# Performance work log

Measured on AMD Instinct MI355X. Metric: run time of the kernel, lower is better.

The kernel has to match this reference:

```python
import jax, jax.numpy as jnp
import numpy as np

BETA = 0.25  # codebook loss weight


def setup_inputs() -> dict:
    key = jax.random.key(0)
    k1, k2 = jax.random.split(key)
    B, C, D = 32768, 4096, 128
    x = jax.random.normal(k1, (B, D), dtype=jnp.float32)
    codes = jax.random.normal(k2, (1, C, D), dtype=jnp.float32)
    return {"x": x, "codes": codes}


def reference(x, codes):
    # x: (B, D), codes: (1, C, D). l2 metric, spherical_norm=False, STE training path
    # (dead-code reinit branch is a no-op on first forward since unused_count==0).
    c = codes[0]  # (C, D)
    x_sq = jnp.sum(x * x, axis=-1, keepdims=True)           # (B, 1)
    c_sq = jnp.sum(c * c, axis=-1)                          # (C,)
    xc = jnp.einsum('bd,cd->bc', x, c)                      # (B, C)
    distances = x_sq + c_sq[None, :] - 2.0 * xc             # (B, C)
    indices = jnp.argmin(distances, axis=-1)                # (B,)
    quantized = c[indices]                                  # (B, D) codebook gather
    # straight-through estimator output
    quantized_out = x + jax.lax.stop_gradient(quantized - x)
    # loss_commit: distance(x, stop_grad(q)); loss_codebook: distance(stop_grad(x), q)
    q_sg = jax.lax.stop_gradient(quantized)
    x_sg = jax.lax.stop_gradient(x)
    loss_commit = jnp.mean(jnp.sum((x - q_sg) ** 2, axis=-1))
    loss_codebook = jnp.mean(jnp.sum((x_sg - quantized) ** 2, axis=-1))
    loss = loss_commit + BETA * loss_codebook
    return quantized_out, indices, loss
```

## Files before the change

kernel.cpp:

```cpp
#include <hip/hip_runtime.h>
#include <float.h>

#define B_ROWS 32768
#define C_CODES 4096
#define DDIM 128
#define MB 128
#define NCHUNKS 4
#define CCHUNK 1024
#define CTILE 64
#define NTILES 16
#define ROWB 256

typedef __attribute__((ext_vector_type(8))) short short8;
typedef __attribute__((ext_vector_type(16))) float f32x16;
using half8 = __attribute__((ext_vector_type(8))) _Float16;
typedef unsigned int u32;
typedef unsigned short u16;
typedef unsigned long long u64;

__device__ __forceinline__ u16 f2h(float f) {
    return __builtin_bit_cast(u16, (_Float16)f);
}

__device__ __forceinline__ void gl2lds16(const void* g, void* l) {
    __builtin_amdgcn_global_load_lds(
        (const __attribute__((address_space(1))) u32*)g,
        (__attribute__((address_space(3))) u32*)l, 16, 0, 0);
}

__global__ void prep_codes(const float* __restrict__ codes, u16* __restrict__ Bbig,
                           float* __restrict__ csqh) {
    const int w = threadIdx.x >> 6, lane = threadIdx.x & 63;
    const int c = blockIdx.x * 4 + w;
    const float2 v = ((const float2*)(codes + (size_t)c * DDIM))[lane];
    ushort2 b; b.x = f2h(v.x); b.y = f2h(v.y);
    const int sw = (c & 15) << 4;
    *(ushort2*)((char*)Bbig + (size_t)c * ROWB + ((lane * 4) ^ sw)) = b;
    float s = v.x * v.x + v.y * v.y;
    #pragma unroll
    for (int off = 32; off; off >>= 1) s += __shfl_xor(s, off);
    if (lane == 0) csqh[c] = 0.5f * s;
}

__global__ void transpose_codes(const float* __restrict__ codes, float* __restrict__ codesT) {
    const int g = blockIdx.x * 256 + threadIdx.x;
    const int d = g & 127;
    const int cg = g >> 7;
    float buf[32];
    #pragma unroll
    for (int k = 0; k < 32; ++k)
        buf[k] = codes[(size_t)(cg * 32 + k) * DDIM + d];
    #pragma unroll
    for (int i = 0; i < 8; ++i) {
        float4 v;
        v.x = buf[i * 4]; v.y = buf[i * 4 + 1]; v.z = buf[i * 4 + 2]; v.w = buf[i * 4 + 3];
        *(float4*)&codesT[(size_t)d * C_CODES + cg * 32 + i * 4] = v;
    }
}

__global__ __launch_bounds__(256, 2)
void gemm_top2(const float* __restrict__ x, const u16* __restrict__ Bbig,
               const float* __restrict__ csqh,
               float* __restrict__ pb1, float* __restrict__ pb2,
               int* __restrict__ pi1, float* __restrict__ xsq_ws) {
    __shared__ char smem[32768 + 4096 + 1024];
    char* const Astage = smem;
    float* const csq_l = (float*)(smem + 32768);
    float* const xsqArr = (float*)(smem + 36864);

    const int tid = threadIdx.x;
    const int lane = tid & 63;
    const int w = tid >> 6;
    const int blkrow = blockIdx.x * MB;
    const int cbase = blockIdx.y * CCHUNK;

    {
        const float4 v = ((const float4*)(csqh + cbase))[tid];
        float4 n; n.x = -v.x; n.y = -v.y; n.z = -v.z; n.w = -v.w;
        ((float4*)csq_l)[tid] = n;
    }
    {
        const int r = tid >> 1, h = tid & 1;
        const float4* xp = (const float4*)(x + (size_t)(blkrow + r) * DDIM + h * 64);
        char* Arow = Astage + r * ROWB;
        const int sw = (r & 15) << 4;
        float ss = 0.f;
        #pragma unroll
        for (int i = 0; i < 16; ++i) {
            const float4 v = xp[i];
            ss += v.x * v.x + v.y * v.y + v.z * v.z + v.w * v.w;
            uint2 pk;
            pk.x = (u32)f2h(v.x) | ((u32)f2h(v.y) << 16);
            pk.y = (u32)f2h(v.z) | ((u32)f2h(v.w) << 16);
            *(uint2*)(Arow + ((h * 128 + i * 8) ^ sw)) = pk;
        }
        xsqArr[tid] = ss;
    }
    __syncthreads();

    const int col0 = lane & 31;
    const int khalf = (lane >> 5) << 4;
    half8 afr[8];
    {
        const int arow = w * 32 + col0;
        const char* Ab = Astage + arow * ROWB;
        const int swa = (arow & 15) << 4;
        #pragma unroll
        for (int ks = 0; ks < 8; ++ks)
            afr[ks] = *(const half8*)(Ab + ((ks * 32 + khalf) ^ swa));
    }
    __syncthreads();

    {
        const char* src = (const char*)Bbig + (size_t)cbase * ROWB;
        #pragma unroll
        for (int r = 0; r < 4; ++r)
            gl2lds16(src + r * 4096 + w * 1024 + lane * 16, smem + r * 4096 + w * 1024);
    }
    __syncthreads();

    float b1v[16], b2v[16]; int b1i[16];
    #pragma unroll
    for (int r = 0; r < 16; ++r) { b1v[r] = -FLT_MAX; b2v[r] = -FLT_MAX; b1i[r] = 0; }

    const int swb = (col0 & 15) << 4;

    for (int t = 0; t < NTILES; ++t) {
        if (t + 1 < NTILES) {
            char* dbuf = smem + ((t + 1) & 1) * 16384;
            const char* src = (const char*)Bbig + (size_t)(cbase + (t + 1) * CTILE) * ROWB;
            #pragma unroll
            for (int r = 0; r < 4; ++r)
                gl2lds16(src + r * 4096 + w * 1024 + lane * 16, dbuf + r * 4096 + w * 1024);
        }
        const char* Bl = smem + (t & 1) * 16384 + col0 * ROWB;

        const float cs0 = csq_l[t * CTILE + col0];
        const float cs1 = csq_l[t * CTILE + 32 + col0];
        f32x16 acc0, acc1;
        #pragma unroll
        for (int i = 0; i < 16; ++i) { acc0[i] = cs0; acc1[i] = cs1; }
        __builtin_amdgcn_s_setprio(1);
        #pragma unroll
        for (int ks = 0; ks < 8; ++ks) {
            const int z = (ks * 32 + khalf) ^ swb;
            const half8 bf0 = *(const half8*)(Bl + z);
            const half8 bf1 = *(const half8*)(Bl + 8192 + z);
            acc0 = __builtin_amdgcn_mfma_f32_32x32x16_f16(afr[ks], bf0, acc0, 0, 0, 0);
            acc1 = __builtin_amdgcn_mfma_f32_32x32x16_f16(afr[ks], bf1, acc1, 0, 0, 0);
        }
        __builtin_amdgcn_s_setprio(0);
        const int idx0 = cbase + t * CTILE + col0;
        const int idx1 = idx0 + 32;
        #pragma unroll
        for (int r = 0; r < 16; ++r) {
            const float s0 = acc0[r];
            const float s1 = acc1[r];
            const float m2a = __builtin_amdgcn_fmed3f(b1v[r], b2v[r], s0);
            const int   nia = (s0 > b1v[r]) ? idx0 : b1i[r];
            const float n1a = fmaxf(b1v[r], s0);
            b2v[r] = __builtin_amdgcn_fmed3f(n1a, m2a, s1);
            b1i[r] = (s1 > n1a) ? idx1 : nia;
            b1v[r] = fmaxf(n1a, s1);
        }
        __syncthreads();
    }

    #pragma unroll
    for (int off = 1; off <= 16; off <<= 1) {
        #pragma unroll
        for (int r = 0; r < 16; ++r) {
            const float o1 = __shfl_xor(b1v[r], off);
            const int   oi = __shfl_xor(b1i[r], off);
            const float o2 = __shfl_xor(b2v[r], off);
            const float lo = fminf(b1v[r], o1);
            const float nb2 = fmaxf(lo, fmaxf(b2v[r], o2));
            const bool take = (o1 > b1v[r]) || (o1 == b1v[r] && oi < b1i[r]);
            if (take) { b1v[r] = o1; b1i[r] = oi; }
            b2v[r] = nb2;
        }
    }
    if (col0 == 0) {
        const int hi = lane >> 5;
        #pragma unroll
        for (int r = 0; r < 16; ++r) {
            const int rloc = w * 32 + (r & 3) + 8 * (r >> 2) + 4 * hi;
            const int grow = blkrow + rloc;
            const size_t o = (size_t)blockIdx.y * B_ROWS + grow;
            pb1[o] = b1v[r]; pb2[o] = b2v[r]; pi1[o] = b1i[r];
            if (blockIdx.y == 0)
                xsq_ws[grow] = xsqArr[2 * rloc] + xsqArr[2 * rloc + 1];
        }
    }
}

__global__ void select_flag(const float* __restrict__ pb1, const float* __restrict__ pb2,
                            const int* __restrict__ pi1, const float* __restrict__ xsq_ws,
                            int* __restrict__ idxf, int* __restrict__ list, int* __restrict__ cnt,
                            u64* __restrict__ amax64) {
    const int r = blockIdx.x * 256 + threadIdx.x;
    float b1 = pb1[r], b2 = pb2[r]; int bi = pi1[r];
    #pragma unroll
    for (int c = 1; c < NCHUNKS; ++c) {
        const float o1 = pb1[(size_t)c * B_ROWS + r], o2 = pb2[(size_t)c * B_ROWS + r];
        const int oi = pi1[(size_t)c * B_ROWS + r];
        const float lo = fminf(b1, o1);
        b2 = fmaxf(lo, fmaxf(b2, o2));
        const bool take = (o1 > b1) || (o1 == b1 && oi < bi);
        if (take) { b1 = o1; bi = oi; }
    }
    idxf[r] = bi;
    const float margin = 0.004f * sqrtf(xsq_ws[r]) + 0.008f;
    const bool flag = (b1 - b2) < margin;
    const unsigned long long m = __ballot(flag);
    const int lane = threadIdx.x & 63;
    int base = 0;
    const int nw = __popcll(m);
    if (lane == 0 && nw) base = atomicAdd(cnt, nw);
    base = __shfl(base, 0);
    if (flag) {
        const int pos = base + (int)__popcll(m & ((1ull << lane) - 1ull));
        list[pos] = r;
        amax64[pos] = 0ull;
    }
}

__global__ __launch_bounds__(256)
void recheck2(const float* __restrict__ x, const float* __restrict__ codesT,
              const float* __restrict__ csqh, const int* __restrict__ list,
              const int* __restrict__ cnt, u64* __restrict__ amax64) {
    __shared__ float xT[128][8];
    __shared__ u64 warr[4][8];
    const int tid = threadIdx.x;
    const int lane = tid & 63, w = tid >> 6;
    const int n = *cnt;
    if (n == 0) return;
    const int ntasks = ((n + 7) >> 3) << 3;

    for (int task = blockIdx.x; task < ntasks; task += gridDim.x) {
        const int slotbase = (task >> 3) << 3;
        const int ch = task & 7;
        __syncthreads();
        #pragma unroll
        for (int k = 0; k < 4; ++k) {
            const int i = tid + k * 256;
            const int d = i & 127, j = i >> 7;
            const int slot = min(slotbase + j, n - 1);
            xT[d][j] = x[(size_t)list[slot] * DDIM + d];
        }
        __syncthreads();

        const int c0 = ch * 512 + tid;
        const int c1 = c0 + 256;
        float acc[2][8][4];
        #pragma unroll
        for (int cc = 0; cc < 2; ++cc)
            #pragma unroll
            for (int r = 0; r < 8; ++r)
                #pragma unroll
                for (int p = 0; p < 4; ++p) acc[cc][r][p] = 0.f;

        for (int d4 = 0; d4 < 32; ++d4) {
            #pragma unroll
            for (int p = 0; p < 4; ++p) {
                const int d = d4 * 4 + p;
                const float cv0 = codesT[(size_t)d * C_CODES + c0];
                const float cv1 = codesT[(size_t)d * C_CODES + c1];
                const float4 xa = *(const float4*)&xT[d][0];
                const float4 xb = *(const float4*)&xT[d][4];
                acc[0][0][p] = fmaf(cv0, xa.x, acc[0][0][p]);
                acc[0][1][p] = fmaf(cv0, xa.y, acc[0][1][p]);
                acc[0][2][p] = fmaf(cv0, xa.z, acc[0][2][p]);
                acc[0][3][p] = fmaf(cv0, xa.w, acc[0][3][p]);
                acc[0][4][p] = fmaf(cv0, xb.x, acc[0][4][p]);
                acc[0][5][p] = fmaf(cv0, xb.y, acc[0][5][p]);
                acc[0][6][p] = fmaf(cv0, xb.z, acc[0][6][p]);
                acc[0][7][p] = fmaf(cv0, xb.w, acc[0][7][p]);
                acc[1][0][p] = fmaf(cv1, xa.x, acc[1][0][p]);
                acc[1][1][p] = fmaf(cv1, xa.y, acc[1][1][p]);
                acc[1][2][p] = fmaf(cv1, xa.z, acc[1][2][p]);
                acc[1][3][p] = fmaf(cv1, xa.w, acc[1][3][p]);
                acc[1][4][p] = fmaf(cv1, xb.x, acc[1][4][p]);
                acc[1][5][p] = fmaf(cv1, xb.y, acc[1][5][p]);
                acc[1][6][p] = fmaf(cv1, xb.z, acc[1][6][p]);
                acc[1][7][p] = fmaf(cv1, xb.w, acc[1][7][p]);
            }
        }

        const float cq0 = csqh[c0], cq1 = csqh[c1];
        #pragma unroll
        for (int r = 0; r < 8; ++r) {
            const float s0 = (acc[0][r][0] + acc[0][r][1]) + (acc[0][r][2] + acc[0][r][3]) - cq0;
            const float s1 = (acc[1][r][0] + acc[1][r][1]) + (acc[1][r][2] + acc[1][r][3]) - cq1;
            const float sb = (s1 > s0) ? s1 : s0;
            const int ib = (s1 > s0) ? c1 : c0;
            u32 su = __float_as_uint(sb);
            su ^= (sb < 0.f) ? 0xFFFFFFFFu : 0x80000000u;
            u64 key = ((u64)su << 32) | (u32)(4095 - ib);
            #pragma unroll
            for (int off = 1; off < 64; off <<= 1) {
                const u64 o = __shfl_xor(key, off);
                key = (o > key) ? o : key;
            }
            if (lane == 0) warr[w][r] = key;
        }
        __syncthreads();
        if (tid < 8) {
            const u64 k01 = warr[0][tid] > warr[1][tid] ? warr[0][tid] : warr[1][tid];
            const u64 k23 = warr[2][tid] > warr[3][tid] ? warr[2][tid] : warr[3][tid];
            const u64 k = k01 > k23 ? k01 : k23;
            atomicMax(&amax64[min(slotbase + tid, n - 1)], k);
        }
    }
}

__global__ void merge_flag(const int* __restrict__ list, const int* __restrict__ cnt,
                           const u64* __restrict__ amax64, int* __restrict__ idxf) {
    const int n = *cnt;
    for (int i = blockIdx.x * 256 + threadIdx.x; i < n; i += gridDim.x * 256)
        idxf[list[i]] = 4095 - (int)(amax64[i] & 0xFFFFFFFFull);
}

__global__ void finalize(const float* __restrict__ x, const float* __restrict__ codes,
                         const int* __restrict__ idxf, float* __restrict__ qout,
                         float* __restrict__ idxout, float* __restrict__ partials) {
    __shared__ float ls[4];
    const int w = threadIdx.x >> 6, lane = threadIdx.x & 63;
    const int rb = blockIdx.x * 16 + w * 4;
    float wsum = 0.f;
    #pragma unroll
    for (int j = 0; j < 4; ++j) {
        const int r = rb + j;
        const int bi = idxf[r];
        const float2 xv = ((const float2*)(x + (size_t)r * DDIM))[lane];
        const float2 cv = ((const float2*)(codes + (size_t)bi * DDIM))[lane];
        ((float2*)(qout + (size_t)r * DDIM))[lane] = cv;
        if (lane == 0) idxout[r] = (float)bi;
        const float dx = xv.x - cv.x, dy = xv.y - cv.y;
        wsum += dx * dx + dy * dy;
    }
    #pragma unroll
    for (int off = 32; off; off >>= 1) wsum += __shfl_xor(wsum, off);
    if (lane == 0) ls[w] = wsum;
    __syncthreads();
    if (threadIdx.x == 0) partials[blockIdx.x] = (ls[0] + ls[1]) + (ls[2] + ls[3]);
}

__global__ void loss_reduce(const float* __restrict__ partials, float* __restrict__ loss) {
    __shared__ float ls[4];
    const int tid = threadIdx.x, w = tid >> 6, lane = tid & 63;
    float s = 0.f;
    for (int i = tid; i < 2048; i += 256) s += partials[i];
    #pragma unroll
    for (int off = 32; off; off >>= 1) s += __shfl_xor(s, off);
    if (lane == 0) ls[w] = s;
    __syncthreads();
    if (tid == 0) *loss = ((ls[0] + ls[1]) + (ls[2] + ls[3])) * (1.25f / (float)B_ROWS);
}

extern "C" void kernel_launch(void* const* d_in, const int* in_sizes, int n_in,
                              void* d_out, int out_size, void* d_ws, size_t ws_size,
                              hipStream_t stream) {
    const float* x = (const float*)d_in[0];
    const float* codes = (const float*)d_in[1];

    float* out = (float*)d_out;
    float* qout = out;
    float* idxout = out + (size_t)B_ROWS * DDIM;
    float* loss = idxout + B_ROWS;

    float* codesT = qout;

    char* ws = (char*)d_ws;
    u16* Bbig     = (u16*)ws;
    float* csqh   = (float*)(ws + 1048576);
    float* pb1    = (float*)(ws + 1064960);
    float* pb2    = (float*)(ws + 1589248);
    int* pi1      = (int*)(ws + 2113536);
    float* xsq_ws = (float*)(ws + 2637824);
    int* idxf     = (int*)(ws + 2768896);
    int* list     = (int*)(ws + 2899968);
    int* cnt      = (int*)(ws + 3031040);
    float* partials = (float*)(ws + 3031168);
    u64* amax64   = (u64*)(ws + 3039360);

    hipMemsetAsync(cnt, 0, 4, stream);
    prep_codes<<<C_CODES / 4, 256, 0, stream>>>(codes, Bbig, csqh);
    transpose_codes<<<64, 256, 0, stream>>>(codes, codesT);
    gemm_top2<<<dim3(B_ROWS / MB, NCHUNKS), 256, 0, stream>>>(x, Bbig, csqh, pb1, pb2, pi1, xsq_ws);
    select_flag<<<B_ROWS / 256, 256, 0, stream>>>(pb1, pb2, pi1, xsq_ws, idxf, list, cnt, amax64);
    recheck2<<<2048, 256, 0, stream>>>(x, codesT, csqh, list, cnt, amax64);
    merge_flag<<<64, 256, 0, stream>>>(list, cnt, amax64, idxf);
    finalize<<<B_ROWS / 16, 256, 0, stream>>>(x, codes, idxf, qout, idxout, partials);
    loss_reduce<<<1, 256, 0, stream>>>(partials, loss);
}
```

Baseline: 129.9 us.

## Deepen GEMM B-tile pipeline to 4 stages and halve codebook chunks

The distance GEMM now walks 32-code half-tiles through a 4-slot LDS ring with prefetch distance 2. It uses explicit vmcnt waits plus raw s_barrier instead of a full __syncthreads per 64-code tile. The codebook is split into 2 chunks of 2048 instead of 4, which halves the partial top-2 writes and the select_flag merge work but also halves grid parallelism. Per-row x-squared partials are written straight to global memory and summed in select_flag, dropping the LDS staging array. Risks are less MFMA interleaving with one accumulator per wave, fewer blocks, and correctness depending on the hand-placed waitcnt counts.

```diff
diff --git a/kernel.cpp b/kernel.cpp
--- a/kernel.cpp
+++ b/kernel.cpp
@@ -5,13 +5,11 @@
 #define C_CODES 4096
 #define DDIM 128
 #define MB 128
-#define NCHUNKS 4
-#define CCHUNK 1024
-#define CTILE 64
-#define NTILES 16
+#define NCHUNKS 2
+#define CCHUNK 2048
+#define NH 64
 #define ROWB 256
 
-typedef __attribute__((ext_vector_type(8))) short short8;
 typedef __attribute__((ext_vector_type(16))) float f32x16;
 using half8 = __attribute__((ext_vector_type(8))) _Float16;
 typedef unsigned int u32;
@@ -62,11 +60,10 @@
 void gemm_top2(const float* __restrict__ x, const u16* __restrict__ Bbig,
                const float* __restrict__ csqh,
                float* __restrict__ pb1, float* __restrict__ pb2,
-               int* __restrict__ pi1, float* __restrict__ xsq_ws) {
-    __shared__ char smem[32768 + 4096 + 1024];
+               int* __restrict__ pi1, float* __restrict__ xsq2) {
+    __shared__ char smem[32768 + 8192];
     char* const Astage = smem;
     float* const csq_l = (float*)(smem + 32768);
-    float* const xsqArr = (float*)(smem + 36864);
 
     const int tid = threadIdx.x;
     const int lane = tid & 63;
@@ -75,9 +72,13 @@
     const int cbase = blockIdx.y * CCHUNK;
 
     {
-        const float4 v = ((const float4*)(csqh + cbase))[tid];
-        float4 n; n.x = -v.x; n.y = -v.y; n.z = -v.z; n.w = -v.w;
-        ((float4*)csq_l)[tid] = n;
+        const float4* cs = (const float4*)(csqh + cbase);
+        #pragma unroll
+        for (int j = 0; j < 2; ++j) {
+            const float4 v = cs[j * 256 + tid];
+            float4 n; n.x = -v.x; n.y = -v.y; n.z = -v.z; n.w = -v.w;
+            ((float4*)csq_l)[j * 256 + tid] = n;
+        }
     }
     {
         const int r = tid >> 1, h = tid & 1;
@@ -94,7 +95,7 @@
             pk.y = (u32)f2h(v.z) | ((u32)f2h(v.w) << 16);
             *(uint2*)(Arow + ((h * 128 + i * 8) ^ sw)) = pk;
         }
-        xsqArr[tid] = ss;
+        if (blockIdx.y == 0) xsq2[blkrow * 2 + tid] = ss;
     }
     __syncthreads();
 
@@ -113,11 +114,13 @@
 
     {
         const char* src = (const char*)Bbig + (size_t)cbase * ROWB;
-        #pragma unroll
-        for (int r = 0; r < 4; ++r)
-            gl2lds16(src + r * 4096 + w * 1024 + lane * 16, smem + r * 4096 + w * 1024);
-    }
-    __syncthreads();
+        gl2lds16(src +         w * 1024 + lane * 16, smem +         w * 1024);
+        gl2lds16(src +  4096 + w * 1024 + lane * 16, smem +  4096 + w * 1024);
+        gl2lds16(src +  8192 + w * 1024 + lane * 16, smem +  8192 + w * 1024);
+        gl2lds16(src + 12288 + w * 1024 + lane * 16, smem + 12288 + w * 1024);
+    }
+    asm volatile("s_waitcnt vmcnt(2)" ::: "memory");
+    __builtin_amdgcn_s_barrier();
 
     float b1v[16], b2v[16]; int b1i[16];
     #pragma unroll
@@ -125,45 +128,38 @@
 
     const int swb = (col0 & 15) << 4;
 
-    for (int t = 0; t < NTILES; ++t) {
-        if (t + 1 < NTILES) {
-            char* dbuf = smem + ((t + 1) & 1) * 16384;
-            const char* src = (const char*)Bbig + (size_t)(cbase + (t + 1) * CTILE) * ROWB;
-            #pragma unroll
-            for (int r = 0; r < 4; ++r)
-                gl2lds16(src + r * 4096 + w * 1024 + lane * 16, dbuf + r * 4096 + w * 1024);
-        }
-        const char* Bl = smem + (t & 1) * 16384 + col0 * ROWB;
-
-        const float cs0 = csq_l[t * CTILE + col0];
-        const float cs1 = csq_l[t * CTILE + 32 + col0];
-        f32x16 acc0, acc1;
-        #pragma unroll
-        for (int i = 0; i < 16; ++i) { acc0[i] = cs0; acc1[i] = cs1; }
+    for (int h = 0; h < NH; ++h) {
+        if (h + 2 < NH) {
+            char* dbuf = smem + ((h + 2) & 3) * 8192;
+            const char* src = (const char*)Bbig + (size_t)(cbase + (h + 2) * 32) * ROWB;
+            gl2lds16(src +        w * 1024 + lane * 16, dbuf +        w * 1024);
+            gl2lds16(src + 4096 + w * 1024 + lane * 16, dbuf + 4096 + w * 1024);
+        }
+        const char* Bl = smem + (h & 3) * 8192 + col0 * ROWB;
+
+        const float cs0 = csq_l[h * 32 + col0];
+        f32x16 acc;
+        #pragma unroll
+        for (int i = 0; i < 16; ++i) acc[i] = cs0;
         __builtin_amdgcn_s_setprio(1);
         #pragma unroll
         for (int ks = 0; ks < 8; ++ks) {
-            const int z = (ks * 32 + khalf) ^ swb;
-            const half8 bf0 = *(const half8*)(Bl + z);
-            const half8 bf1 = *(const half8*)(Bl + 8192 + z);
-            acc0 = __builtin_amdgcn_mfma_f32_32x32x16_f16(afr[ks], bf0, acc0, 0, 0, 0);
-            acc1 = __builtin_amdgcn_mfma_f32_32x32x16_f16(afr[ks], bf1, acc1, 0, 0, 0);
+            const half8 bf = *(const half8*)(Bl + ((ks * 32 + khalf) ^ swb));
+            acc = __builtin_amdgcn_mfma_f32_32x32x16_f16(afr[ks], bf, acc, 0, 0, 0);
         }
         __builtin_amdgcn_s_setprio(0);
-        const int idx0 = cbase + t * CTILE + col0;
-        const int idx1 = idx0 + 32;
+        const int idx0 = cbase + h * 32 + col0;
         #pragma unroll
         for (int r = 0; r < 16; ++r) {
-            const float s0 = acc0[r];
-            const float s1 = acc1[r];
-            const float m2a = __builtin_amdgcn_fmed3f(b1v[r], b2v[r], s0);
-            const int   nia = (s0 > b1v[r]) ? idx0 : b1i[r];
-            const float n1a = fmaxf(b1v[r], s0);
-            b2v[r] = __builtin_amdgcn_fmed3f(n1a, m2a, s1);
-            b1i[r] = (s1 > n1a) ? idx1 : nia;
-            b1v[r] = fmaxf(n1a, s1);
-        }
-        __syncthreads();
+            const float s0 = acc[r];
+            const float m2 = __builtin_amdgcn_fmed3f(b1v[r], b2v[r], s0);
+            b1i[r] = (s0 > b1v[r]) ? idx0 : b1i[r];
+            b1v[r] = fmaxf(b1v[r], s0);
+            b2v[r] = m2;
+        }
+        if (h + 2 < NH) { asm volatile("s_waitcnt vmcnt(2)" ::: "memory"); }
+        else            { asm volatile("s_waitcnt vmcnt(0)" ::: "memory"); }
+        __builtin_amdgcn_s_barrier();
     }
 
     #pragma unroll
@@ -188,14 +184,12 @@
             const int grow = blkrow + rloc;
             const size_t o = (size_t)blockIdx.y * B_ROWS + grow;
             pb1[o] = b1v[r]; pb2[o] = b2v[r]; pi1[o] = b1i[r];
-            if (blockIdx.y == 0)
-                xsq_ws[grow] = xsqArr[2 * rloc] + xsqArr[2 * rloc + 1];
         }
     }
 }
 
 __global__ void select_flag(const float* __restrict__ pb1, const float* __restrict__ pb2,
-                            const int* __restrict__ pi1, const float* __restrict__ xsq_ws,
+                            const int* __restrict__ pi1, const float* __restrict__ xsq2,
                             int* __restrict__ idxf, int* __restrict__ list, int* __restrict__ cnt,
                             u64* __restrict__ amax64) {
     const int r = blockIdx.x * 256 + threadIdx.x;
@@ -210,7 +204,8 @@
         if (take) { b1 = o1; bi = oi; }
     }
     idxf[r] = bi;
-    const float margin = 0.004f * sqrtf(xsq_ws[r]) + 0.008f;
+    const float xsq = xsq2[2 * r] + xsq2[2 * r + 1];
+    const float margin = 0.004f * sqrtf(xsq) + 0.008f;
     const bool flag = (b1 - b2) < margin;
     const unsigned long long m = __ballot(flag);
     const int lane = threadIdx.x & 63;
@@ -375,20 +370,20 @@
     u16* Bbig     = (u16*)ws;
     float* csqh   = (float*)(ws + 1048576);
     float* pb1    = (float*)(ws + 1064960);
-    float* pb2    = (float*)(ws + 1589248);
-    int* pi1      = (int*)(ws + 2113536);
-    float* xsq_ws = (float*)(ws + 2637824);
-    int* idxf     = (int*)(ws + 2768896);
-    int* list     = (int*)(ws + 2899968);
-    int* cnt      = (int*)(ws + 3031040);
-    float* partials = (float*)(ws + 3031168);
-    u64* amax64   = (u64*)(ws + 3039360);
+    float* pb2    = (float*)(ws + 1327104);
+    int* pi1      = (int*)(ws + 1589248);
+    float* xsq2   = (float*)(ws + 1851392);
+    int* idxf     = (int*)(ws + 2113536);
+    int* list     = (int*)(ws + 2244608);
+    int* cnt      = (int*)(ws + 2375680);
+    float* partials = (float*)(ws + 2375808);
+    u64* amax64   = (u64*)(ws + 2384000);
 
     hipMemsetAsync(cnt, 0, 4, stream);
     prep_codes<<<C_CODES / 4, 256, 0, stream>>>(codes, Bbig, csqh);
     transpose_codes<<<64, 256, 0, stream>>>(codes, codesT);
-    gemm_top2<<<dim3(B_ROWS / MB, NCHUNKS), 256, 0, stream>>>(x, Bbig, csqh, pb1, pb2, pi1, xsq_ws);
-    select_flag<<<B_ROWS / 256, 256, 0, stream>>>(pb1, pb2, pi1, xsq_ws, idxf, list, cnt, amax64);
+    gemm_top2<<<dim3(B_ROWS / MB, NCHUNKS), 256, 0, stream>>>(x, Bbig, csqh, pb1, pb2, pi1, xsq2);
+    select_flag<<<B_ROWS / 256, 256, 0, stream>>>(pb1, pb2, pi1, xsq2, idxf, list, cnt, amax64);
     recheck2<<<2048, 256, 0, stream>>>(x, codesT, csqh, list, cnt, amax64);
     merge_flag<<<64, 256, 0, stream>>>(list, cnt, amax64, idxf);
     finalize<<<B_ROWS / 16, 256, 0, stream>>>(x, codes, idxf, qout, idxout, partials);
```

New measurement: 120.4 us. -7.3%, faster.

## Precompute fp16 swizzled x once in fused prep kernel; async-load it in GEMM

Applied to the files above, without the earlier changes.

Merges prep_codes, transpose_codes and a new x-to-fp16 conversion into one launch. The conversion writes swizzled fp16 rows and per-half squared norms into scratch space inside the output buffer. gemm_top2 then streams the pre-converted A tile into LDS with global_load_lds instead of reading fp32 x and converting it in each of the 4 chunk blocks. This removes repeated conversion work and a kernel launch, but adds an extra global write and read of the fp16 x (8 MB) and places scratch data in the output region, which later kernels must overwrite.

```diff
diff --git a/kernel.cpp b/kernel.cpp
--- a/kernel.cpp
+++ b/kernel.cpp
@@ -11,7 +11,6 @@
 #define NTILES 16
 #define ROWB 256
 
-typedef __attribute__((ext_vector_type(8))) short short8;
 typedef __attribute__((ext_vector_type(16))) float f32x16;
 using half8 = __attribute__((ext_vector_type(8))) _Float16;
 typedef unsigned int u32;
@@ -28,61 +27,41 @@
         (__attribute__((address_space(3))) u32*)l, 16, 0, 0);
 }
 
-__global__ void prep_codes(const float* __restrict__ codes, u16* __restrict__ Bbig,
-                           float* __restrict__ csqh) {
-    const int w = threadIdx.x >> 6, lane = threadIdx.x & 63;
-    const int c = blockIdx.x * 4 + w;
-    const float2 v = ((const float2*)(codes + (size_t)c * DDIM))[lane];
-    ushort2 b; b.x = f2h(v.x); b.y = f2h(v.y);
-    const int sw = (c & 15) << 4;
-    *(ushort2*)((char*)Bbig + (size_t)c * ROWB + ((lane * 4) ^ sw)) = b;
-    float s = v.x * v.x + v.y * v.y;
-    #pragma unroll
-    for (int off = 32; off; off >>= 1) s += __shfl_xor(s, off);
-    if (lane == 0) csqh[c] = 0.5f * s;
-}
-
-__global__ void transpose_codes(const float* __restrict__ codes, float* __restrict__ codesT) {
-    const int g = blockIdx.x * 256 + threadIdx.x;
-    const int d = g & 127;
-    const int cg = g >> 7;
-    float buf[32];
-    #pragma unroll
-    for (int k = 0; k < 32; ++k)
-        buf[k] = codes[(size_t)(cg * 32 + k) * DDIM + d];
-    #pragma unroll
-    for (int i = 0; i < 8; ++i) {
-        float4 v;
-        v.x = buf[i * 4]; v.y = buf[i * 4 + 1]; v.z = buf[i * 4 + 2]; v.w = buf[i * 4 + 3];
-        *(float4*)&codesT[(size_t)d * C_CODES + cg * 32 + i * 4] = v;
-    }
-}
-
-__global__ __launch_bounds__(256, 2)
-void gemm_top2(const float* __restrict__ x, const u16* __restrict__ Bbig,
-               const float* __restrict__ csqh,
-               float* __restrict__ pb1, float* __restrict__ pb2,
-               int* __restrict__ pi1, float* __restrict__ xsq_ws) {
-    __shared__ char smem[32768 + 4096 + 1024];
-    char* const Astage = smem;
-    float* const csq_l = (float*)(smem + 32768);
-    float* const xsqArr = (float*)(smem + 36864);
-
+__global__ void prep_fused(const float* __restrict__ codes, const float* __restrict__ x,
+                           u16* __restrict__ Bbig, float* __restrict__ csqh,
+                           float* __restrict__ codesT, u16* __restrict__ Axf16,
+                           float* __restrict__ xsq2) {
     const int tid = threadIdx.x;
-    const int lane = tid & 63;
-    const int w = tid >> 6;
-    const int blkrow = blockIdx.x * MB;
-    const int cbase = blockIdx.y * CCHUNK;
-
-    {
-        const float4 v = ((const float4*)(csqh + cbase))[tid];
-        float4 n; n.x = -v.x; n.y = -v.y; n.z = -v.z; n.w = -v.w;
-        ((float4*)csq_l)[tid] = n;
-    }
-    {
-        const int r = tid >> 1, h = tid & 1;
-        const float4* xp = (const float4*)(x + (size_t)(blkrow + r) * DDIM + h * 64);
-        char* Arow = Astage + r * ROWB;
+    if (blockIdx.x < C_CODES / 4) {
+        const int w = tid >> 6, lane = tid & 63;
+        const int c = blockIdx.x * 4 + w;
+        const float2 v = ((const float2*)(codes + (size_t)c * DDIM))[lane];
+        ushort2 b; b.x = f2h(v.x); b.y = f2h(v.y);
+        const int sw = (c & 15) << 4;
+        *(ushort2*)((char*)Bbig + (size_t)c * ROWB + ((lane * 4) ^ sw)) = b;
+        float s = v.x * v.x + v.y * v.y;
+        #pragma unroll
+        for (int off = 32; off; off >>= 1) s += __shfl_xor(s, off);
+        if (lane == 0) csqh[c] = 0.5f * s;
+    } else if (blockIdx.x < C_CODES / 4 + 64) {
+        const int g = (blockIdx.x - C_CODES / 4) * 256 + tid;
+        const int d = g & 127;
+        const int cg = g >> 7;
+        float buf[32];
+        #pragma unroll
+        for (int k = 0; k < 32; ++k)
+            buf[k] = codes[(size_t)(cg * 32 + k) * DDIM + d];
+        #pragma unroll
+        for (int i = 0; i < 8; ++i) {
+            float4 v;
+            v.x = buf[i * 4]; v.y = buf[i * 4 + 1]; v.z = buf[i * 4 + 2]; v.w = buf[i * 4 + 3];
+            *(float4*)&codesT[(size_t)d * C_CODES + cg * 32 + i * 4] = v;
+        }
+    } else {
+        const int xb = blockIdx.x - (C_CODES / 4 + 64);
+        const int r = xb * 128 + (tid >> 1), h = tid & 1;
+        const float4* xp = (const float4*)(x + (size_t)r * DDIM + h * 64);
+        char* Arow = (char*)Axf16 + (size_t)r * ROWB;
         const int sw = (r & 15) << 4;
         float ss = 0.f;
         #pragma unroll
@@ -94,7 +73,34 @@
             pk.y = (u32)f2h(v.z) | ((u32)f2h(v.w) << 16);
             *(uint2*)(Arow + ((h * 128 + i * 8) ^ sw)) = pk;
         }
-        xsqArr[tid] = ss;
+        xsq2[(size_t)r * 2 + h] = ss;
+    }
+}
+
+__global__ __launch_bounds__(256, 2)
+void gemm_top2(const u16* __restrict__ Axf16, const u16* __restrict__ Bbig,
+               const float* __restrict__ csqh,
+               float* __restrict__ pb1, float* __restrict__ pb2,
+               int* __restrict__ pi1) {
+    __shared__ char smem[32768 + 4096];
+    float* const csq_l = (float*)(smem + 32768);
+
+    const int tid = threadIdx.x;
+    const int lane = tid & 63;
+    const int w = tid >> 6;
+    const int blkrow = blockIdx.x * MB;
+    const int cbase = blockIdx.y * CCHUNK;
+
+    {
+        const float4 v = ((const float4*)(csqh + cbase))[tid];
+        float4 n; n.x = -v.x; n.y = -v.y; n.z = -v.z; n.w = -v.w;
+        ((float4*)csq_l)[tid] = n;
+    }
+    {
+        const char* src = (const char*)Axf16 + (size_t)blkrow * ROWB;
+        #pragma unroll
+        for (int j = 0; j < 8; ++j)
+            gl2lds16(src + j * 4096 + tid * 16, smem + j * 4096 + tid * 16);
     }
     __syncthreads();
 
@@ -103,7 +109,7 @@
     half8 afr[8];
     {
         const int arow = w * 32 + col0;
-        const char* Ab = Astage + arow * ROWB;
+        const char* Ab = smem + arow * ROWB;
         const int swa = (arow & 15) << 4;
         #pragma unroll
         for (int ks = 0; ks < 8; ++ks)
@@ -188,14 +194,12 @@
             const int grow = blkrow + rloc;
             const size_t o = (size_t)blockIdx.y * B_ROWS + grow;
             pb1[o] = b1v[r]; pb2[o] = b2v[r]; pi1[o] = b1i[r];
-            if (blockIdx.y == 0)
-                xsq_ws[grow] = xsqArr[2 * rloc] + xsqArr[2 * rloc + 1];
         }
     }
 }
 
 __global__ void select_flag(const float* __restrict__ pb1, const float* __restrict__ pb2,
-                            const int* __restrict__ pi1, const float* __restrict__ xsq_ws,
+                            const int* __restrict__ pi1, const float* __restrict__ xsq2,
                             int* __restrict__ idxf, int* __restrict__ list, int* __restrict__ cnt,
                             u64* __restrict__ amax64) {
     const int r = blockIdx.x * 256 + threadIdx.x;
@@ -210,7 +214,8 @@
         if (take) { b1 = o1; bi = oi; }
     }
     idxf[r] = bi;
-    const float margin = 0.004f * sqrtf(xsq_ws[r]) + 0.008f;
+    const float xsq = xsq2[2 * r] + xsq2[2 * r + 1];
+    const float margin = 0.004f * sqrtf(xsq) + 0.008f;
     const bool flag = (b1 - b2) < margin;
     const unsigned long long m = __ballot(flag);
     const int lane = threadIdx.x & 63;
@@ -370,6 +375,7 @@
     float* loss = idxout + B_ROWS;
 
     float* codesT = qout;
+    u16* Axf16 = (u16*)(qout + 524288);
 
     char* ws = (char*)d_ws;
     u16* Bbig     = (u16*)ws;
@@ -377,18 +383,18 @@
     float* pb1    = (float*)(ws + 1064960);
     float* pb2    = (float*)(ws + 1589248);
     int* pi1      = (int*)(ws + 2113536);
-    float* xsq_ws = (float*)(ws + 2637824);
-    int* idxf     = (int*)(ws + 2768896);
-    int* list     = (int*)(ws + 2899968);
-    int* cnt      = (int*)(ws + 3031040);
-    float* partials = (float*)(ws + 3031168);
-    u64* amax64   = (u64*)(ws + 3039360);
+    float* xsq2   = (float*)(ws + 2637824);
+    int* idxf     = (int*)(ws + 2899968);
+    int* list     = (int*)(ws + 3031040);
+    int* cnt      = (int*)(ws + 3162112);
+    float* partials = (float*)(ws + 3162240);
+    u64* amax64   = (u64*)(ws + 3170432);
 
     hipMemsetAsync(cnt, 0, 4, stream);
-    prep_codes<<<C_CODES / 4, 256, 0, stream>>>(codes, Bbig, csqh);
-    transpose_codes<<<64, 256, 0, stream>>>(codes, codesT);
-    gemm_top2<<<dim3(B_ROWS / MB, NCHUNKS), 256, 0, stream>>>(x, Bbig, csqh, pb1, pb2, pi1, xsq_ws);
-    select_flag<<<B_ROWS / 256, 256, 0, stream>>>(pb1, pb2, pi1, xsq_ws, idxf, list, cnt, amax64);
+    prep_fused<<<C_CODES / 4 + 64 + B_ROWS / 128, 256, 0, stream>>>(
+        codes, x, Bbig, csqh, codesT, Axf16, xsq2);
+    gemm_top2<<<dim3(B_ROWS / MB, NCHUNKS), 256, 0, stream>>>(Axf16, Bbig, csqh, pb1, pb2, pi1);
+    select_flag<<<B_ROWS / 256, 256, 0, stream>>>(pb1, pb2, pi1, xsq2, idxf, list, cnt, amax64);
     recheck2<<<2048, 256, 0, stream>>>(x, codesT, csqh, list, cnt, amax64);
     merge_flag<<<64, 256, 0, stream>>>(list, cnt, amax64, idxf);
     finalize<<<B_ROWS / 16, 256, 0, stream>>>(x, codes, idxf, qout, idxout, partials);
```

Measured after the change: 130.8 us. Within noise of the previous version (+0.7%).
